# Kernel tuning notes

Hardware: AMD Instinct MI355X
Metric: run time of the kernel (lower is better)

Reference implementation:

```python
import jax, jax.numpy as jnp
import numpy as np

N = 8192          # batch of labeled text embeddings
D = 256           # embedding dim
NUM_LABELS = 128  # distinct cluster labels


def setup_inputs() -> dict:
    key = jax.random.key(0)
    k1, k2 = jax.random.split(key)
    embeddings = jax.random.normal(k1, (N, D), dtype=jnp.float32)
    labels = jax.random.randint(k2, (N,), 0, NUM_LABELS, dtype=jnp.int64)
    logit_scale = jnp.array([20.0], dtype=jnp.float32)  # 1 / temperature, temperature=0.05
    return {"embeddings": embeddings, "labels": labels, "logit_scale": logit_scale}


def reference(embeddings, labels, logit_scale):
    # Equivalent reformulation of the per-group python loop:
    # for each label group g with >=2 members,
    #   contribution = (sum_{j!=k in g} exp(-s*sim_jk)) * (sum_{j in g, l not in g} exp(s*sim_jl))
    # loss = log(1 + sum_g contribution)
    s = logit_scale[0]
    eps = 1e-12  # matches torch F.normalize clamp
    e = embeddings / jnp.maximum(jnp.linalg.norm(embeddings, axis=1, keepdims=True), eps)
    S = (e @ e.T) * s                                   # [N, N] scaled cosine similarity
    n = labels.shape[0]
    same = labels[:, None] == labels[None, :]           # [N, N] same-label mask
    offdiag = ~jnp.eye(n, dtype=bool)
    pos_mask = same & offdiag                           # same label, j != k
    neg_mask = ~same                                    # different label
    # per-row partial sums (fused exp+mask+reduce under jit)
    a = jnp.sum(jnp.exp(-S) * pos_mask, axis=1)         # [N] positive-pair terms
    b = jnp.sum(jnp.exp(S) * neg_mask, axis=1)          # [N] negative-pair terms
    # aggregate per label group
    counts = jax.ops.segment_sum(jnp.ones((n,), dtype=jnp.float32), labels, num_segments=NUM_LABELS)
    A = jax.ops.segment_sum(a, labels, num_segments=NUM_LABELS)
    B = jax.ops.segment_sum(b, labels, num_segments=NUM_LABELS)
    valid = counts >= 2.0                               # groups with <2 members are skipped
    sum_value = 1.0 + jnp.sum(jnp.where(valid, A * B, 0.0))
    return jnp.log(sum_value)
```

## Files before the change

kernel.cpp:

```cpp
#include <hip/hip_runtime.h>
#include <hip/hip_bf16.h>
#include <math.h>


typedef __attribute__((ext_vector_type(2))) long l2;
typedef __attribute__((ext_vector_type(4))) float f32x4;

#define N_EMB 8192
#define D_EMB 256
#define NUM_LABELS 128
#define PAN 128
#define NPAN (N_EMB / PAN)
#define NTRI (NPAN * (NPAN + 1) / 2)
#define NSLOT 128

template <int CTRL>
__device__ __forceinline__ float dpp_add(float x) {
    int y = __builtin_amdgcn_update_dpp(0, __builtin_bit_cast(int, x),
                                        CTRL, 0xF, 0xF, false);
    return x + __builtin_bit_cast(float, y);
}
__device__ __forceinline__ float red16(float x) {
    x = dpp_add<0xB1>(x);
    x = dpp_add<0x4E>(x);
    x = dpp_add<0x124>(x);
    x = dpp_add<0x128>(x);
    return x;
}

__device__ __forceinline__ float exp2hw(float x) {
    float r;
    asm("v_exp_f32 %0, %1" : "=v"(r) : "v"(x));
    return r;
}

__global__ __launch_bounds__(256) void normalize_kernel(const float* __restrict__ emb,
                                                        char* __restrict__ e8,
                                                        float* __restrict__ slots) {
    const int wid = threadIdx.x >> 6, lane = threadIdx.x & 63;
    const int row = blockIdx.x * 4 + wid;
    const f32x4 x = *(const f32x4*)(emb + (size_t)row * D_EMB + lane * 4);
    float ss = x[0]*x[0] + x[1]*x[1] + x[2]*x[2] + x[3]*x[3];
    #pragma unroll
    for (int off = 32; off >= 1; off >>= 1) ss += __shfl_xor(ss, off);
    const float r = 1.0f / fmaxf(sqrtf(ss), 1e-12f);
    int v = __builtin_amdgcn_cvt_pk_fp8_f32(x[0] * r, x[1] * r, 0, false);
    v = __builtin_amdgcn_cvt_pk_fp8_f32(x[2] * r, x[3] * r, v, true);
    const int u    = lane >> 4;
    const int half = (lane >> 3) & 1;
    const int lp   = ((lane >> 1) & 3) * 16 + (row & 15);
    const int j0   = (lane & 1) * 4;
    char* dst = e8 + ((size_t)(row >> 4) * 4 + u) * 1024 + lp * 16 + half * 8 + j0;
    *(unsigned*)dst = (unsigned)v;
    if (blockIdx.x < NSLOT) slots[blockIdx.x * 256 + threadIdx.x] = 0.f;
}

#define LOADF(dst, voff, sb, OFFSTR) \
    asm volatile("global_load_dwordx4 %0, %1, %2 offset:" OFFSTR \
                 : "=v"(dst) : "v"(voff), "s"(sb))

#define ISSUE(PA_, PB_, OFFSTR) \
    LOADF(PA_[0], voA[0], sbA, OFFSTR); LOADF(PA_[1], voA[1], sbA, OFFSTR); \
    LOADF(PA_[2], voA[2], sbA, OFFSTR); LOADF(PA_[3], voA[3], sbA, OFFSTR); \
    LOADF(PB_[0], voB[0], sbB, OFFSTR); LOADF(PB_[1], voB[1], sbB, OFFSTR); \
    LOADF(PB_[2], voB[2], sbB, OFFSTR); LOADF(PB_[3], voB[3], sbB, OFFSTR)

#define WAITV(NSTR) \
    asm volatile("s_waitcnt vmcnt(" NSTR ")" ::: "memory"); \
    __builtin_amdgcn_sched_barrier(0)

#define MF8(a, b, c) __builtin_amdgcn_mfma_f32_16x16x32_fp8_fp8(a, b, c, 0, 0, 0)

#define MROW(PA_, PB_, mi, H) \
    acc[mi][0] = MF8(PA_[mi][H], PB_[0][H], acc[mi][0]); \
    acc[mi][1] = MF8(PA_[mi][H], PB_[1][H], acc[mi][1]); \
    acc[mi][2] = MF8(PA_[mi][H], PB_[2][H], acc[mi][2]); \
    acc[mi][3] = MF8(PA_[mi][H], PB_[3][H], acc[mi][3]);

#define MFMA32(PA_, PB_) \
    __builtin_amdgcn_s_setprio(1); \
    MROW(PA_, PB_, 0, 0) MROW(PA_, PB_, 1, 0) MROW(PA_, PB_, 2, 0) MROW(PA_, PB_, 3, 0) \
    MROW(PA_, PB_, 0, 1) MROW(PA_, PB_, 1, 1) MROW(PA_, PB_, 2, 1) MROW(PA_, PB_, 3, 1) \
    __builtin_amdgcn_s_setprio(0)

__global__ __launch_bounds__(256, 3) void cosent_main(const char* __restrict__ e8,
                                                      const int* __restrict__ labels,
                                                      const float* __restrict__ scale,
                                                      float* __restrict__ slots) {
    __shared__ float rowsc[2][PAN][2];
    __shared__ float colsc[2][PAN][2];
    __shared__ float binA[NUM_LABELS], binB[NUM_LABELS];
    __shared__ int labR[PAN], labC[PAN];

    const int bid = blockIdx.x;
    const int swz = (bid & 7) * 260 + (bid >> 3);
    int by = (int)((129.0f - sqrtf(16641.0f - 8.0f * (float)swz)) * 0.5f);
    by = by < 0 ? 0 : (by > 63 ? 63 : by);
    while (by < 63 && (by + 1) * (129 - (by + 1)) / 2 <= swz) ++by;
    while (by > 0 && by * (129 - by) / 2 > swz) --by;
    const int bx = by + (swz - by * (129 - by) / 2);
    const bool diag = (bx == by);
    const int rowBase = by * PAN, colBase = bx * PAN;

    const int tid = threadIdx.x, lane = tid & 63, wid = tid >> 6;
    const int wm = wid >> 1, wn = wid & 1;
    const int rr = lane & 15, kh = lane >> 4;

    if (tid < PAN) { labR[tid] = labels[rowBase + tid]; binA[tid] = 0.f; binB[tid] = 0.f; }
    else           { labC[tid - PAN] = labels[colBase + tid - PAN]; }

    const int laneB = lane * 16;
    int voA[4], voB[4];
    #pragma unroll
    for (int i = 0; i < 4; ++i) {
        voA[i] = (wm * 4 + i) * 4096 + laneB;
        voB[i] = (wn * 4 + i) * 4096 + laneB;
    }
    const char* sbA = e8 + (size_t)rowBase * 256;
    const char* sbB = e8 + (size_t)colBase * 256;

    f32x4 acc[4][4];
    #pragma unroll
    for (int i = 0; i < 4; ++i)
        #pragma unroll
        for (int j = 0; j < 4; ++j) acc[i][j] = (f32x4){0.f, 0.f, 0.f, 0.f};

    l2 pA[4], pB[4], qA[4], qB[4];

    ISSUE(pA, pB, "0");
    ISSUE(qA, qB, "1024"); WAITV("8"); MFMA32(pA, pB);
    ISSUE(pA, pB, "2048"); WAITV("8"); MFMA32(qA, qB);
    ISSUE(qA, qB, "3072"); WAITV("8"); MFMA32(pA, pB);
    WAITV("0"); MFMA32(qA, qB);

    __syncthreads();

    const float s2 = *scale * 1.44269504088896f;
    int lc[4];
    #pragma unroll
    for (int ni = 0; ni < 4; ++ni) lc[ni] = labC[wn * 64 + ni * 16 + rr];
    float colA[4] = {0.f, 0.f, 0.f, 0.f}, colB[4] = {0.f, 0.f, 0.f, 0.f};

    #pragma unroll
    for (int mi = 0; mi < 4; ++mi) {
        #pragma unroll
        for (int r = 0; r < 4; ++r) {
            const int rowL = wm * 64 + mi * 16 + kh * 4 + r;
            const int lr = labR[rowL];
            float asum = 0.f, bsum = 0.f;
            #pragma unroll
            for (int ni = 0; ni < 4; ++ni) {
                const int colL = wn * 64 + ni * 16 + rr;
                const float val = acc[mi][ni][r] * s2;
                const bool pos = (lr == lc[ni]);
                float ex = exp2hw(pos ? -val : val);
                if (diag && rowL == colL) ex = 0.f;
                if (pos) { asum += ex; colA[ni] += ex; }
                else     { bsum += ex; colB[ni] += ex; }
            }
            asum = red16(asum);
            bsum = red16(bsum);
            if (rr == 0) { rowsc[wn][rowL][0] = asum; rowsc[wn][rowL][1] = bsum; }
        }
    }

    if (!diag) {
        #pragma unroll
        for (int ni = 0; ni < 4; ++ni) {
            float a = colA[ni], b = colB[ni];
            a += __shfl_xor(a, 16); a += __shfl_xor(a, 32);
            b += __shfl_xor(b, 16); b += __shfl_xor(b, 32);
            if (lane < 16) {
                colsc[wm][wn * 64 + ni * 16 + lane][0] = a;
                colsc[wm][wn * 64 + ni * 16 + lane][1] = b;
            }
        }
    }
    __syncthreads();

    if (tid < PAN) {
        const float ra = rowsc[0][tid][0] + rowsc[1][tid][0];
        const float rb = rowsc[0][tid][1] + rowsc[1][tid][1];
        atomicAdd(&binA[labR[tid]], ra);
        atomicAdd(&binB[labR[tid]], rb);
        if (!diag) {
            const float ca = colsc[0][tid][0] + colsc[1][tid][0];
            const float cb = colsc[0][tid][1] + colsc[1][tid][1];
            atomicAdd(&binA[labC[tid]], ca);
            atomicAdd(&binB[labC[tid]], cb);
        }
    }
    __syncthreads();

    if (tid < NUM_LABELS) {
        float* slot = slots + (size_t)(bid & (NSLOT - 1)) * (NUM_LABELS * 2);
        const float a = binA[tid], b = binB[tid];
        if (a != 0.f) atomicAdd(&slot[tid * 2 + 0], a);
        if (b != 0.f) atomicAdd(&slot[tid * 2 + 1], b);
    }
}

__global__ __launch_bounds__(256) void finalize_kernel(const float* __restrict__ slots,
                                                       const int* __restrict__ labels,
                                                       float* __restrict__ out) {
    __shared__ int cnt[NUM_LABELS];
    __shared__ float w2[4];
    const int tid = threadIdx.x;
    if (tid < NUM_LABELS) cnt[tid] = 0;
    __syncthreads();
    for (int i = tid; i < N_EMB; i += 256) atomicAdd(&cnt[labels[i]], 1);
    __syncthreads();

    float A = 0.f, B = 0.f;
    if (tid < NUM_LABELS) {
        #pragma unroll 8
        for (int s = 0; s < NSLOT; ++s) {
            const float* p = slots + (size_t)s * (NUM_LABELS * 2) + tid * 2;
            A += p[0]; B += p[1];
        }
    }
    float v = (tid < NUM_LABELS && cnt[tid] >= 2) ? A * B : 0.f;
    #pragma unroll
    for (int off = 32; off >= 1; off >>= 1) v += __shfl_xor(v, off);
    if ((tid & 63) == 0) w2[tid >> 6] = v;
    __syncthreads();
    if (tid == 0) out[0] = logf(1.0f + w2[0] + w2[1] + w2[2] + w2[3]);
}

extern "C" void kernel_launch(void* const* d_in, const int* in_sizes, int n_in,
                              void* d_out, int out_size, void* d_ws, size_t ws_size,
                              hipStream_t stream) {
    const float* emb    = (const float*)d_in[0];
    const int*   labels = (const int*)d_in[1];
    const float* scale  = (const float*)d_in[2];
    float* out = (float*)d_out;

    char*  e8    = (char*)d_ws;
    float* slots = (float*)((char*)d_ws + (size_t)N_EMB * D_EMB);

    normalize_kernel<<<N_EMB / 4, 256, 0, stream>>>(emb, e8, slots);
    cosent_main<<<NTRI, 256, 0, stream>>>(e8, labels, scale, slots);
    finalize_kernel<<<1, 256, 0, stream>>>(slots, labels, out);
}
```

Measured before the change: 52.61 us.

## Split loss into label-free all-pairs sum plus per-group correction tiles

The main tile pass no longer looks up labels. It computes the plain exp(sim) sum over all pairs, with the scale folded into the fp8 embeddings, and writes per-row partials to a panel array instead of doing shared and global atomics. A separate set of 128 blocks gathers each label group through a counting-sort list and uses bf16 MFMA to compute the exact positive-pair terms A and the same-group exp(+s) correction subtracted from the total. Two new kernels (list build and row reduce) are added, and groups larger than PCAP=192 would be truncated. Folding the scale into fp8 values also changes quantization error, and the subtraction may lose precision.

```diff
diff --git a/kernel.cpp b/kernel.cpp
--- a/kernel.cpp
+++ b/kernel.cpp
@@ -5,6 +5,7 @@
 
 typedef __attribute__((ext_vector_type(2))) long l2;
 typedef __attribute__((ext_vector_type(4))) float f32x4;
+typedef __attribute__((ext_vector_type(8))) __bf16 bf16x8;
 
 #define N_EMB 8192
 #define D_EMB 256
@@ -12,7 +13,7 @@
 #define PAN 128
 #define NPAN (N_EMB / PAN)
 #define NTRI (NPAN * (NPAN + 1) / 2)
-#define NSLOT 128
+#define PCAP 192
 
 template <int CTRL>
 __device__ __forceinline__ float dpp_add(float x) {
@@ -34,9 +35,19 @@
     return r;
 }
 
+__device__ __forceinline__ unsigned packbf(float a, float b) {
+    unsigned ua = __builtin_bit_cast(unsigned, a);
+    unsigned ub = __builtin_bit_cast(unsigned, b);
+    ua += 0x7FFFu + ((ua >> 16) & 1u);
+    ub += 0x7FFFu + ((ub >> 16) & 1u);
+    return (ua >> 16) | (ub & 0xFFFF0000u);
+}
+
 __global__ __launch_bounds__(256) void normalize_kernel(const float* __restrict__ emb,
+                                                        const float* __restrict__ scale,
                                                         char* __restrict__ e8,
-                                                        float* __restrict__ slots) {
+                                                        unsigned* __restrict__ e16,
+                                                        int* __restrict__ cnt) {
     const int wid = threadIdx.x >> 6, lane = threadIdx.x & 63;
     const int row = blockIdx.x * 4 + wid;
     const f32x4 x = *(const f32x4*)(emb + (size_t)row * D_EMB + lane * 4);
@@ -44,15 +55,30 @@
     #pragma unroll
     for (int off = 32; off >= 1; off >>= 1) ss += __shfl_xor(ss, off);
     const float r = 1.0f / fmaxf(sqrtf(ss), 1e-12f);
-    int v = __builtin_amdgcn_cvt_pk_fp8_f32(x[0] * r, x[1] * r, 0, false);
-    v = __builtin_amdgcn_cvt_pk_fp8_f32(x[2] * r, x[3] * r, v, true);
+    const float ps = sqrtf(scale[0] * 1.44269504088896f) * r;
+
+    int v = __builtin_amdgcn_cvt_pk_fp8_f32(x[0] * ps, x[1] * ps, 0, false);
+    v = __builtin_amdgcn_cvt_pk_fp8_f32(x[2] * ps, x[3] * ps, v, true);
     const int u    = lane >> 4;
     const int half = (lane >> 3) & 1;
     const int lp   = ((lane >> 1) & 3) * 16 + (row & 15);
     const int j0   = (lane & 1) * 4;
     char* dst = e8 + ((size_t)(row >> 4) * 4 + u) * 1024 + lp * 16 + half * 8 + j0;
     *(unsigned*)dst = (unsigned)v;
-    if (blockIdx.x < NSLOT) slots[blockIdx.x * 256 + threadIdx.x] = 0.f;
+
+    uint2 o = { packbf(x[0] * r, x[1] * r), packbf(x[2] * r, x[3] * r) };
+    *(uint2*)((char*)e16 + (size_t)row * 512 + lane * 8) = o;
+
+    if (blockIdx.x == 0 && threadIdx.x < NUM_LABELS) cnt[threadIdx.x] = 0;
+}
+
+__global__ __launch_bounds__(256) void build_lists(const int* __restrict__ labels,
+                                                   int* __restrict__ cnt,
+                                                   int* __restrict__ perm) {
+    const int i = blockIdx.x * 256 + threadIdx.x;
+    const int g = labels[i];
+    const int slot = atomicAdd(&cnt[g], 1);
+    if (slot < PCAP) perm[g * PCAP + slot] = i;
 }
 
 #define LOADF(dst, voff, sb, OFFSTR) \
@@ -84,15 +110,67 @@
     __builtin_amdgcn_s_setprio(0)
 
 __global__ __launch_bounds__(256, 3) void cosent_main(const char* __restrict__ e8,
-                                                      const int* __restrict__ labels,
+                                                      const __bf16* __restrict__ e16,
+                                                      const int* __restrict__ perm,
+                                                      const int* __restrict__ cnt,
                                                       const float* __restrict__ scale,
-                                                      float* __restrict__ slots) {
-    __shared__ float rowsc[2][PAN][2];
-    __shared__ float colsc[2][PAN][2];
-    __shared__ float binA[NUM_LABELS], binB[NUM_LABELS];
-    __shared__ int labR[PAN], labC[PAN];
-
-    const int bid = blockIdx.x;
+                                                      float* __restrict__ wsT,
+                                                      float* __restrict__ Acorr,
+                                                      float* __restrict__ Pcorr) {
+    __shared__ float rowsc[2][PAN];
+    __shared__ float colsc[2][PAN];
+    __shared__ int ilist[PCAP];
+    __shared__ float wredA[4], wredP[4];
+
+    const int tid = threadIdx.x, lane = tid & 63, wid = tid >> 6;
+    const int rr = lane & 15, kh = lane >> 4;
+
+    if (blockIdx.x < NUM_LABELS) {
+        const int g = blockIdx.x;
+        const int c = cnt[g];
+        if (tid < c && tid < PCAP) ilist[tid] = perm[g * PCAP + tid];
+        __syncthreads();
+        const float s2 = scale[0] * 1.44269504088896f;
+        const int nt = (c + 15) >> 4;
+        float pa = 0.f, pp = 0.f;
+        for (int tt = wid; tt < nt * nt; tt += 4) {
+            const int ti = tt / nt, tj = tt - ti * nt;
+            const int rloc = ti * 16 + rr, cloc = tj * 16 + rr;
+            const int ridx = ilist[rloc < c ? rloc : 0];
+            const int cidx = ilist[cloc < c ? cloc : 0];
+            f32x4 a4 = (f32x4){0.f, 0.f, 0.f, 0.f};
+            #pragma unroll
+            for (int t = 0; t < 8; ++t) {
+                const bf16x8 af = *(const bf16x8*)(e16 + (size_t)ridx * 256 + t * 32 + kh * 8);
+                const bf16x8 bf = *(const bf16x8*)(e16 + (size_t)cidx * 256 + t * 32 + kh * 8);
+                a4 = __builtin_amdgcn_mfma_f32_16x16x32_bf16(af, bf, a4, 0, 0, 0);
+            }
+            #pragma unroll
+            for (int r = 0; r < 4; ++r) {
+                const int rg = ti * 16 + kh * 4 + r;
+                const int cg = tj * 16 + rr;
+                const bool in = (rg < c) && (cg < c);
+                const int rj = ilist[in ? rg : 0];
+                const int rk = ilist[in ? cg : 0];
+                const float v = a4[r] * s2;
+                if (in && rj != rk) { pa += exp2hw(-v); pp += exp2hw(v); }
+            }
+        }
+        #pragma unroll
+        for (int off = 32; off >= 1; off >>= 1) {
+            pa += __shfl_xor(pa, off);
+            pp += __shfl_xor(pp, off);
+        }
+        if (lane == 0) { wredA[wid] = pa; wredP[wid] = pp; }
+        __syncthreads();
+        if (tid == 0) {
+            Acorr[g] = wredA[0] + wredA[1] + wredA[2] + wredA[3];
+            Pcorr[g] = wredP[0] + wredP[1] + wredP[2] + wredP[3];
+        }
+        return;
+    }
+
+    const int bid = blockIdx.x - NUM_LABELS;
     const int swz = (bid & 7) * 260 + (bid >> 3);
     int by = (int)((129.0f - sqrtf(16641.0f - 8.0f * (float)swz)) * 0.5f);
     by = by < 0 ? 0 : (by > 63 ? 63 : by);
@@ -102,12 +180,7 @@
     const bool diag = (bx == by);
     const int rowBase = by * PAN, colBase = bx * PAN;
 
-    const int tid = threadIdx.x, lane = tid & 63, wid = tid >> 6;
     const int wm = wid >> 1, wn = wid & 1;
-    const int rr = lane & 15, kh = lane >> 4;
-
-    if (tid < PAN) { labR[tid] = labels[rowBase + tid]; binA[tid] = 0.f; binB[tid] = 0.f; }
-    else           { labC[tid - PAN] = labels[colBase + tid - PAN]; }
 
     const int laneB = lane * 16;
     int voA[4], voB[4];
@@ -133,98 +206,89 @@
     ISSUE(qA, qB, "3072"); WAITV("8"); MFMA32(pA, pB);
     WAITV("0"); MFMA32(qA, qB);
 
-    __syncthreads();
-
-    const float s2 = *scale * 1.44269504088896f;
-    int lc[4];
-    #pragma unroll
-    for (int ni = 0; ni < 4; ++ni) lc[ni] = labC[wn * 64 + ni * 16 + rr];
-    float colA[4] = {0.f, 0.f, 0.f, 0.f}, colB[4] = {0.f, 0.f, 0.f, 0.f};
-
-    #pragma unroll
-    for (int mi = 0; mi < 4; ++mi) {
-        #pragma unroll
-        for (int r = 0; r < 4; ++r) {
-            const int rowL = wm * 64 + mi * 16 + kh * 4 + r;
-            const int lr = labR[rowL];
-            float asum = 0.f, bsum = 0.f;
+    float colT[4] = {0.f, 0.f, 0.f, 0.f};
+    if (!diag) {
+        #pragma unroll
+        for (int mi = 0; mi < 4; ++mi) {
             #pragma unroll
-            for (int ni = 0; ni < 4; ++ni) {
-                const int colL = wn * 64 + ni * 16 + rr;
-                const float val = acc[mi][ni][r] * s2;
-                const bool pos = (lr == lc[ni]);
-                float ex = exp2hw(pos ? -val : val);
-                if (diag && rowL == colL) ex = 0.f;
-                if (pos) { asum += ex; colA[ni] += ex; }
-                else     { bsum += ex; colB[ni] += ex; }
+            for (int r = 0; r < 4; ++r) {
+                float bs = 0.f;
+                #pragma unroll
+                for (int ni = 0; ni < 4; ++ni) {
+                    const float ex = exp2hw(acc[mi][ni][r]);
+                    bs += ex;
+                    colT[ni] += ex;
+                }
+                bs = red16(bs);
+                if (rr == 0) rowsc[wn][wm * 64 + mi * 16 + kh * 4 + r] = bs;
             }
-            asum = red16(asum);
-            bsum = red16(bsum);
-            if (rr == 0) { rowsc[wn][rowL][0] = asum; rowsc[wn][rowL][1] = bsum; }
-        }
-    }
-
-    if (!diag) {
+        }
         #pragma unroll
         for (int ni = 0; ni < 4; ++ni) {
-            float a = colA[ni], b = colB[ni];
+            float a = colT[ni];
             a += __shfl_xor(a, 16); a += __shfl_xor(a, 32);
-            b += __shfl_xor(b, 16); b += __shfl_xor(b, 32);
-            if (lane < 16) {
-                colsc[wm][wn * 64 + ni * 16 + lane][0] = a;
-                colsc[wm][wn * 64 + ni * 16 + lane][1] = b;
+            if (lane < 16) colsc[wm][wn * 64 + ni * 16 + lane] = a;
+        }
+    } else {
+        #pragma unroll
+        for (int mi = 0; mi < 4; ++mi) {
+            #pragma unroll
+            for (int r = 0; r < 4; ++r) {
+                const int rowL = wm * 64 + mi * 16 + kh * 4 + r;
+                float bs = 0.f;
+                #pragma unroll
+                for (int ni = 0; ni < 4; ++ni) {
+                    float ex = exp2hw(acc[mi][ni][r]);
+                    if (rowL == wn * 64 + ni * 16 + rr) ex = 0.f;
+                    bs += ex;
+                }
+                bs = red16(bs);
+                if (rr == 0) rowsc[wn][rowL] = bs;
             }
         }
     }
     __syncthreads();
 
     if (tid < PAN) {
-        const float ra = rowsc[0][tid][0] + rowsc[1][tid][0];
-        const float rb = rowsc[0][tid][1] + rowsc[1][tid][1];
-        atomicAdd(&binA[labR[tid]], ra);
-        atomicAdd(&binB[labR[tid]], rb);
-        if (!diag) {
-            const float ca = colsc[0][tid][0] + colsc[1][tid][0];
-            const float cb = colsc[0][tid][1] + colsc[1][tid][1];
-            atomicAdd(&binA[labC[tid]], ca);
-            atomicAdd(&binB[labC[tid]], cb);
-        }
+        wsT[(size_t)bx * N_EMB + rowBase + tid] = rowsc[0][tid] + rowsc[1][tid];
+        if (!diag)
+            wsT[(size_t)by * N_EMB + colBase + tid] = colsc[0][tid] + colsc[1][tid];
     }
+}
+
+__global__ __launch_bounds__(256) void reduce_rows(const float* __restrict__ wsT,
+                                                   const int* __restrict__ labels,
+                                                   float* __restrict__ part) {
+    __shared__ float Tb[NUM_LABELS];
+    const int tid = threadIdx.x;
+    if (tid < NUM_LABELS) Tb[tid] = 0.f;
     __syncthreads();
-
-    if (tid < NUM_LABELS) {
-        float* slot = slots + (size_t)(bid & (NSLOT - 1)) * (NUM_LABELS * 2);
-        const float a = binA[tid], b = binB[tid];
-        if (a != 0.f) atomicAdd(&slot[tid * 2 + 0], a);
-        if (b != 0.f) atomicAdd(&slot[tid * 2 + 1], b);
-    }
-}
-
-__global__ __launch_bounds__(256) void finalize_kernel(const float* __restrict__ slots,
-                                                       const int* __restrict__ labels,
+    const int row = blockIdx.x * 256 + tid;
+    float t = 0.f;
+    #pragma unroll
+    for (int p = 0; p < NPAN; ++p) t += wsT[(size_t)p * N_EMB + row];
+    atomicAdd(&Tb[labels[row]], t);
+    __syncthreads();
+    if (tid < NUM_LABELS) part[blockIdx.x * NUM_LABELS + tid] = Tb[tid];
+}
+
+__global__ __launch_bounds__(128) void finalize_kernel(const float* __restrict__ part,
+                                                       const float* __restrict__ Acorr,
+                                                       const float* __restrict__ Pcorr,
+                                                       const int* __restrict__ cnt,
                                                        float* __restrict__ out) {
-    __shared__ int cnt[NUM_LABELS];
-    __shared__ float w2[4];
-    const int tid = threadIdx.x;
-    if (tid < NUM_LABELS) cnt[tid] = 0;
+    const int g = threadIdx.x;
+    float T = 0.f;
+    #pragma unroll 8
+    for (int b = 0; b < 32; ++b) T += part[b * NUM_LABELS + g];
+    const float B = T - Pcorr[g];
+    float v = (cnt[g] >= 2) ? Acorr[g] * B : 0.f;
+    #pragma unroll
+    for (int off = 32; off >= 1; off >>= 1) v += __shfl_xor(v, off);
+    __shared__ float w2[2];
+    if ((g & 63) == 0) w2[g >> 6] = v;
     __syncthreads();
-    for (int i = tid; i < N_EMB; i += 256) atomicAdd(&cnt[labels[i]], 1);
-    __syncthreads();
-
-    float A = 0.f, B = 0.f;
-    if (tid < NUM_LABELS) {
-        #pragma unroll 8
-        for (int s = 0; s < NSLOT; ++s) {
-            const float* p = slots + (size_t)s * (NUM_LABELS * 2) + tid * 2;
-            A += p[0]; B += p[1];
-        }
-    }
-    float v = (tid < NUM_LABELS && cnt[tid] >= 2) ? A * B : 0.f;
-    #pragma unroll
-    for (int off = 32; off >= 1; off >>= 1) v += __shfl_xor(v, off);
-    if ((tid & 63) == 0) w2[tid >> 6] = v;
-    __syncthreads();
-    if (tid == 0) out[0] = logf(1.0f + w2[0] + w2[1] + w2[2] + w2[3]);
+    if (g == 0) out[0] = logf(1.0f + w2[0] + w2[1]);
 }
 
 extern "C" void kernel_launch(void* const* d_in, const int* in_sizes, int n_in,
@@ -235,10 +299,20 @@
     const float* scale  = (const float*)d_in[2];
     float* out = (float*)d_out;
 
-    char*  e8    = (char*)d_ws;
-    float* slots = (float*)((char*)d_ws + (size_t)N_EMB * D_EMB);
-
-    normalize_kernel<<<N_EMB / 4, 256, 0, stream>>>(emb, e8, slots);
-    cosent_main<<<NTRI, 256, 0, stream>>>(e8, labels, scale, slots);
-    finalize_kernel<<<1, 256, 0, stream>>>(slots, labels, out);
-}
+    char* base = (char*)d_ws;
+    char*     e8    = base;
+    unsigned* e16   = (unsigned*)(base + (2u << 20));
+    float*    wsT   = (float*)(base + (6u << 20));
+    int*      cnt   = (int*)(base + (8u << 20));
+    int*      perm  = (int*)(base + (8u << 20) + 1024);
+    float*    Acorr = (float*)(base + (8u << 20) + 112 * 1024);
+    float*    Pcorr = Acorr + NUM_LABELS;
+    float*    part  = Pcorr + NUM_LABELS;
+
+    normalize_kernel<<<N_EMB / 4, 256, 0, stream>>>(emb, scale, e8, e16, cnt);
+    build_lists<<<N_EMB / 256, 256, 0, stream>>>(labels, cnt, perm);
+    cosent_main<<<NTRI + NUM_LABELS, 256, 0, stream>>>(e8, (const __bf16*)e16, perm,
+                                                       cnt, scale, wsT, Acorr, Pcorr);
+    reduce_rows<<<N_EMB / 256, 256, 0, stream>>>(wsT, labels, part);
+    finalize_kernel<<<1, 128, 0, stream>>>(part, Acorr, Pcorr, cnt, out);
+}
```

Result: slower. 65.28 us (+24.1%).
